# Kernel optimization log

Hardware: AMD Instinct MI355X
Metric: run time of the kernel (lower is better)

The kernel has to match this reference:

```python
import jax, jax.numpy as jnp
import numpy as np

BS, NPTS, NM, D = 8, 8192, 32, 512  # objects, points/object, masks/object, feature dim


def setup_inputs() -> dict:
    key = jax.random.key(0)
    k1, k2, k3 = jax.random.split(key, 3)
    net_out = jax.random.normal(k1, (BS * NPTS, D), dtype=jnp.float32)
    mask_embs = jax.random.normal(k2, (BS * NM, D), dtype=jnp.float32)
    mask_pts = (jax.random.uniform(k3, (BS, NM, NPTS)) < 0.5).astype(jnp.float32)
    pt_offset = (jnp.arange(1, BS + 1) * NPTS).astype(jnp.int32)  # per-object end idx
    logit_scale = jnp.float32(2.6593)  # ln(1/0.07), CLIP-style
    return {
        "net_out": net_out,
        "mask_embs": mask_embs,
        "mask_pts": mask_pts,
        "logit_scale": logit_scale,
        "pt_offset": pt_offset,
    }


def reference(net_out, mask_embs, mask_pts, logit_scale, pt_offset):
    bs, nm, npts = mask_pts.shape
    d = net_out.shape[1]
    n_total = bs * nm

    # ragged per-object mask_pt @ net_out[start:end] -> uniform batched matmul
    net = net_out.reshape(bs, npts, d)
    sum_feats = jnp.einsum('bmp,bpd->bmd', mask_pts, net).reshape(n_total, d)

    mask_npts = jnp.sum(mask_pts, axis=-1).reshape(n_total, 1)  # points per mask
    nopts = (mask_npts[:, 0] == 0)                              # empty masks -> ignored
    avg_feats = sum_feats / (mask_npts + 1e-12)

    logits = (mask_embs @ avg_feats.T) * jnp.exp(logit_scale)   # [N, N]

    idx = jnp.arange(n_total)
    valid = ~nopts  # target == -100 (ignore) for empty masks, else arange diagonal
    texts_loss = jnp.where(valid, -jax.nn.log_softmax(logits, axis=-1)[idx, idx], 0.0)
    pts_loss = jnp.where(valid, -jax.nn.log_softmax(logits.T, axis=-1)[idx, idx], 0.0)

    def nonzero_avg(l):
        cnt = jnp.sum(l > 0)
        return jnp.where(cnt > 0, jnp.sum(l) / jnp.maximum(cnt, 1), 0.0)

    return (nonzero_avg(texts_loss) + nonzero_avg(pts_loss)) / 2.0
```

## Files before the change

### kernel.cpp

```cpp
#include <hip/hip_runtime.h>
#include <hip/hip_bf16.h>
#include <math.h>

#define BS 8
#define NPTS 8192
#define NM 32
#define D 512
#define NT (BS*NM)
#define KC 32
#define KCHUNK (NPTS/KC)
#define TILES (KCHUNK/32)
#define DC 8
#define DCHUNK (D/DC)
#define NWORDS (NPTS/32)

#define LOG2E 1.44269504088896f
#define LN2   0.69314718055995f

typedef short short8 __attribute__((ext_vector_type(8)));
typedef float f32x4 __attribute__((ext_vector_type(4)));

static constexpr size_t OFF_SUMF = 0;
static constexpr size_t OFF_CNTS = OFF_SUMF + (size_t)NT*D;
static constexpr size_t OFF_BITS = OFF_CNTS + NT;
static constexpr size_t OFF_LOG  = OFF_BITS + (size_t)NT*NWORDS;
static constexpr size_t OFF_RLSE = OFF_LOG + (size_t)NT*NT;
static constexpr size_t OFF_CLSE = OFF_RLSE + NT;
static constexpr size_t OFF_TICK = OFF_CLSE + NT;

__device__ __forceinline__ short bf16_rne(float f) {
  return __builtin_bit_cast(short, __float2bfloat16(f));
}

#define GLOAD_LDS16(g, l) __builtin_amdgcn_global_load_lds( \
    (const __attribute__((address_space(1))) void*)(g),     \
    (__attribute__((address_space(3))) void*)(l), 16, 0, 0)

__global__ __launch_bounds__(256) void kp_prep(const float* __restrict__ mpts,
                                               unsigned int* __restrict__ mbits,
                                               float* __restrict__ cnts,
                                               float* __restrict__ sumf,
                                               int* __restrict__ ticket) {
  const int n = blockIdx.x;
  const int t = threadIdx.x;
  if (n == 0 && t == 0) *ticket = 0;
  const float4* mp = (const float4*)(mpts + ((size_t)n << 13) + t * 32);
  unsigned int u = 0;
  #pragma unroll
  for (int q = 0; q < 8; ++q) {
    const float4 v = mp[q];
    u |= (v.x != 0.f ? 1u : 0u) << (q * 4 + 0);
    u |= (v.y != 0.f ? 1u : 0u) << (q * 4 + 1);
    u |= (v.z != 0.f ? 1u : 0u) << (q * 4 + 2);
    u |= (v.w != 0.f ? 1u : 0u) << (q * 4 + 3);
  }
  mbits[n * NWORDS + t] = u;
  ((float2*)(sumf + ((size_t)n << 9)))[t] = make_float2(0.f, 0.f);
  int c = __popc(u);
  #pragma unroll
  for (int o = 32; o > 0; o >>= 1) c += __shfl_down(c, o, 64);
  __shared__ int red[4];
  if ((t & 63) == 0) red[t >> 6] = c;
  __syncthreads();
  if (t == 0) cnts[n] = (float)(red[0] + red[1] + red[2] + red[3]);
}

__global__ __launch_bounds__(256, 8) void k1_mfma(const float* __restrict__ net,
                                                  const unsigned int* __restrict__ mbits,
                                                  float* __restrict__ sumf) {
  __shared__ float tile[2][32 * DCHUNK];
  const int bx = blockIdx.x;
  const int dc = bx & 7;
  const int kc = (bx >> 3) & 31;
  const int b  = bx >> 8;
  const int w    = threadIdx.x >> 6;
  const int lane = threadIdx.x & 63;
  const int lhi = lane >> 4, llo = lane & 15;
  const int k0 = kc * KCHUNK;

  auto stage = [&](int buf, int t) {
    const int kt = k0 + t * 32;
    #pragma unroll
    for (int si = 0; si < 2; ++si) {
      const int s = w * 2 + si;
      const int gsrc = (lane & 15) ^ (((s >> 1) & 3) << 2);
      const float* src = net
        + (((size_t)(b * NPTS + kt + s * 4 + (lane >> 4))) << 9)
        + dc * DCHUNK + (gsrc << 2);
      GLOAD_LDS16(src, &tile[buf][s * 256]);
    }
  };

  const unsigned int* r0 = mbits + (size_t)(b * NM + llo) * NWORDS + kc * TILES;
  const unsigned int* r1 = r0 + (size_t)16 * NWORDS;

  f32x4 acc0 = {0.f, 0.f, 0.f, 0.f};
  f32x4 acc1 = {0.f, 0.f, 0.f, 0.f};

  const int rbase = (lhi * 8) * 64 + ((((w * 4) + (llo >> 2)) ^ (lhi << 2)) << 2) + (llo & 3);
  const int sh = lhi * 8;

  stage(0, 0);
  __syncthreads();

  #pragma unroll
  for (int t = 0; t < TILES; ++t) {
    const int cur = t & 1;
    const unsigned int u0 = r0[t];
    const unsigned int u1 = r1[t];
    if (t + 1 < TILES) stage(cur ^ 1, t + 1);

    float bv[8];
    #pragma unroll
    for (int j = 0; j < 8; ++j) bv[j] = tile[cur][rbase + j * 64];

    short8 bf, a0f, a1f;
    #pragma unroll
    for (int j = 0; j < 8; ++j) bf[j] = bf16_rne(bv[j]);
    const unsigned int b0 = (u0 >> sh) & 0xffu;
    const unsigned int b1 = (u1 >> sh) & 0xffu;
    #pragma unroll
    for (int j = 0; j < 8; ++j) {
      a0f[j] = (short)(-(int)((b0 >> j) & 1u) & 0x3F80);
      a1f[j] = (short)(-(int)((b1 >> j) & 1u) & 0x3F80);
    }

    acc0 = __builtin_amdgcn_mfma_f32_16x16x32_bf16(a0f, bf, acc0, 0, 0, 0);
    acc1 = __builtin_amdgcn_mfma_f32_16x16x32_bf16(a1f, bf, acc1, 0, 0, 0);

    __syncthreads();
  }

  const int d0 = dc * DCHUNK + w * 16;
  float* sp = sumf + (((size_t)(b * NM)) << 9) + d0 + llo;
  #pragma unroll
  for (int j = 0; j < 4; ++j) {
    atomicAdd(sp + ((size_t)(lhi * 4 + j) << 9),      acc0[j]);
    atomicAdd(sp + ((size_t)(16 + lhi * 4 + j) << 9), acc1[j]);
  }
}

__global__ __launch_bounds__(128) void k2_logits(const float* __restrict__ embs,
                                                 const float* __restrict__ sumf,
                                                 const float* __restrict__ cnts,
                                                 const float* __restrict__ lsc,
                                                 float* __restrict__ logits) {
  const int h = threadIdx.x >> 6;
  const int lane = threadIdx.x & 63;
  const int wt = blockIdx.x;
  const int ti = wt >> 4, tj = wt & 15;
  const int lhi = lane >> 4, llo = lane & 15;

  const float* ea = embs + (((size_t)(ti * 16 + llo)) << 9) + h * 256 + lhi * 8;
  const float* sv = sumf + (((size_t)(tj * 16 + llo)) << 9) + h * 256 + lhi * 8;
  f32x4 acc = {0.f, 0.f, 0.f, 0.f};
  #pragma unroll
  for (int kk = 0; kk < 8; ++kk) {
    const float4 e0 = *(const float4*)(ea);
    const float4 e1 = *(const float4*)(ea + 4);
    const float4 v0 = *(const float4*)(sv);
    const float4 v1 = *(const float4*)(sv + 4);
    const float ev[8] = {e0.x, e0.y, e0.z, e0.w, e1.x, e1.y, e1.z, e1.w};
    const float vv[8] = {v0.x, v0.y, v0.z, v0.w, v1.x, v1.y, v1.z, v1.w};
    short8 ef, vf;
    #pragma unroll
    for (int j = 0; j < 8; ++j) { ef[j] = bf16_rne(ev[j]); vf[j] = bf16_rne(vv[j]); }
    acc = __builtin_amdgcn_mfma_f32_16x16x32_bf16(ef, vf, acc, 0, 0, 0);
    ea += 32; sv += 32;
  }

  __shared__ float part[64 * 4];
  if (h == 1) *(float4*)(&part[lane * 4]) = make_float4(acc[0], acc[1], acc[2], acc[3]);
  __syncthreads();
  if (h == 0) {
    const float4 p = *(const float4*)(&part[lane * 4]);
    const float scale = expf(lsc[0]);
    const float invc = scale / (cnts[tj * 16 + llo] + 1e-12f);
    float* lp = logits + (size_t)(ti * 16) * NT + tj * 16 + llo;
    lp[(size_t)(lhi * 4 + 0) * NT] = (acc[0] + p.x) * invc;
    lp[(size_t)(lhi * 4 + 1) * NT] = (acc[1] + p.y) * invc;
    lp[(size_t)(lhi * 4 + 2) * NT] = (acc[2] + p.z) * invc;
    lp[(size_t)(lhi * 4 + 3) * NT] = (acc[3] + p.w) * invc;
  }
}

__global__ __launch_bounds__(256) void k3_lse(const float* __restrict__ logits,
                                              float* __restrict__ rowlse,
                                              float* __restrict__ clse,
                                              const float* __restrict__ cnts,
                                              int* __restrict__ ticket,
                                              float* __restrict__ out) {
  const int g = blockIdx.x;
  const int r = threadIdx.x >> 4;
  const int c = threadIdx.x & 15;
  __shared__ float red[16][17];
  if (g < 16) {
    const int col = g * 16 + c;
    float mx = -1e30f;
    #pragma unroll 4
    for (int kk = 0; kk < 16; ++kk)
      mx = fmaxf(mx, logits[(size_t)(kk * 16 + r) * NT + col]);
    red[r][c] = mx; __syncthreads();
    for (int st = 8; st; st >>= 1) { if (r < st) red[r][c] = fmaxf(red[r][c], red[r + st][c]); __syncthreads(); }
    const float mx2 = red[0][c] * LOG2E; __syncthreads();
    float s = 0.f;
    #pragma unroll 4
    for (int kk = 0; kk < 16; ++kk)
      s += exp2f(logits[(size_t)(kk * 16 + r) * NT + col] * LOG2E - mx2);
    red[r][c] = s; __syncthreads();
    for (int st = 8; st; st >>= 1) { if (r < st) red[r][c] += red[r + st][c]; __syncthreads(); }
    if (r == 0) clse[col] = (mx2 + log2f(red[0][c])) * LN2;
  } else {
    const int row = (g - 16) * 16 + r;
    float mx = -1e30f;
    #pragma unroll 4
    for (int kk = 0; kk < 16; ++kk)
      mx = fmaxf(mx, logits[(size_t)row * NT + kk * 16 + c]);
    #pragma unroll
    for (int o = 8; o; o >>= 1) mx = fmaxf(mx, __shfl_xor(mx, o, 64));
    const float mx2 = mx * LOG2E;
    float s = 0.f;
    #pragma unroll 4
    for (int kk = 0; kk < 16; ++kk)
      s += exp2f(logits[(size_t)row * NT + kk * 16 + c] * LOG2E - mx2);
    #pragma unroll
    for (int o = 8; o; o >>= 1) s += __shfl_xor(s, o, 64);
    if (c == 0) rowlse[row] = (mx2 + log2f(s)) * LN2;
  }

  __shared__ int slast;
  __syncthreads();
  if (threadIdx.x == 0) {
    __threadfence();
    slast = (atomicAdd(ticket, 1) == 31);
  }
  __syncthreads();
  if (!slast) return;
  __threadfence();

  const int i = threadIdx.x;
  const float diag = logits[(size_t)i * NT + i];
  const bool valid = cnts[i] > 0.f;
  const float tl = valid ? (rowlse[i] - diag) : 0.f;
  const float pl = valid ? (clse[i] - diag) : 0.f;

  __shared__ float fred[4][256];
  fred[0][i] = tl;
  fred[1][i] = (tl > 0.f) ? 1.f : 0.f;
  fred[2][i] = pl;
  fred[3][i] = (pl > 0.f) ? 1.f : 0.f;
  __syncthreads();
  for (int st = 128; st > 0; st >>= 1) {
    if (i < st) {
      fred[0][i] += fred[0][i + st];
      fred[1][i] += fred[1][i + st];
      fred[2][i] += fred[2][i + st];
      fred[3][i] += fred[3][i + st];
    }
    __syncthreads();
  }
  if (i == 0) {
    const float a1 = (fred[1][0] > 0.f) ? fred[0][0] / fmaxf(fred[1][0], 1.f) : 0.f;
    const float a2 = (fred[3][0] > 0.f) ? fred[2][0] / fmaxf(fred[3][0], 1.f) : 0.f;
    out[0] = 0.5f * (a1 + a2);
  }
}

extern "C" void kernel_launch(void* const* d_in, const int* in_sizes, int n_in,
                              void* d_out, int out_size, void* d_ws, size_t ws_size,
                              hipStream_t stream) {
  const float* net  = (const float*)d_in[0];
  const float* embs = (const float*)d_in[1];
  const float* mpts = (const float*)d_in[2];
  const float* lsc  = (const float*)d_in[3];

  float* ws     = (float*)d_ws;
  float* sumf   = ws + OFF_SUMF;
  float* cnts   = ws + OFF_CNTS;
  unsigned int* mbits = (unsigned int*)(ws + OFF_BITS);
  float* logits = ws + OFF_LOG;
  float* rowlse = ws + OFF_RLSE;
  float* clse   = ws + OFF_CLSE;
  int*   ticket = (int*)(ws + OFF_TICK);
  float* outp   = (float*)d_out;

  kp_prep<<<dim3(NT), dim3(256), 0, stream>>>(mpts, mbits, cnts, sumf, ticket);
  k1_mfma<<<dim3(BS * KC * DC), dim3(256), 0, stream>>>(net, mbits, sumf);
  k2_logits<<<dim3(NT), dim3(128), 0, stream>>>(embs, sumf, cnts, lsc, logits);
  k3_lse<<<dim3(32), dim3(256), 0, stream>>>(logits, rowlse, clse, cnts, ticket, outp);
}
```

Measured before the change: 51.95 us.

## Triple-buffer k1 LDS staging with vmcnt waits and ballot-based mask packing

The matmul kernel moves from double to triple buffering of the LDS tiles. It uses explicit s_waitcnt vmcnt plus a single barrier per iteration, replacing two __syncthreads, so global-to-LDS loads run two tiles ahead. Each lane's 8 mask words are preloaded with vector loads before the loop, and the occupancy hint drops from 8 to 6 to fit the larger LDS footprint. The prep kernel now packs mask bits with wave ballots over coalesced scalar loads instead of per-thread float4 loops, producing the same bit layout.

New measurement: 56.50 us. +8.8%, slower.

```diff
diff --git a/kernel.cpp b/kernel.cpp
--- a/kernel.cpp
+++ b/kernel.cpp
@@ -43,32 +43,31 @@
                                                int* __restrict__ ticket) {
   const int n = blockIdx.x;
   const int t = threadIdx.x;
+  const int w = t >> 6, lane = t & 63;
   if (n == 0 && t == 0) *ticket = 0;
-  const float4* mp = (const float4*)(mpts + ((size_t)n << 13) + t * 32);
-  unsigned int u = 0;
-  #pragma unroll
-  for (int q = 0; q < 8; ++q) {
-    const float4 v = mp[q];
-    u |= (v.x != 0.f ? 1u : 0u) << (q * 4 + 0);
-    u |= (v.y != 0.f ? 1u : 0u) << (q * 4 + 1);
-    u |= (v.z != 0.f ? 1u : 0u) << (q * 4 + 2);
-    u |= (v.w != 0.f ? 1u : 0u) << (q * 4 + 3);
-  }
-  mbits[n * NWORDS + t] = u;
+
+  const float* base = mpts + ((size_t)n << 13) + w * 2048;
+  uint2* wout = (uint2*)(mbits + (size_t)n * NWORDS + w * 64);
+  int cnt = 0;
+  #pragma unroll 8
+  for (int i = 0; i < 32; ++i) {
+    const float v = base[i * 64 + lane];
+    const unsigned long long m = __ballot(v != 0.f);
+    cnt += __popcll(m);
+    if (lane == 0) wout[i] = make_uint2((unsigned)m, (unsigned)(m >> 32));
+  }
+  __shared__ float redc[4];
+  if (lane == 0) redc[w] = (float)cnt;
+  __syncthreads();
+  if (t == 0) cnts[n] = redc[0] + redc[1] + redc[2] + redc[3];
+
   ((float2*)(sumf + ((size_t)n << 9)))[t] = make_float2(0.f, 0.f);
-  int c = __popc(u);
-  #pragma unroll
-  for (int o = 32; o > 0; o >>= 1) c += __shfl_down(c, o, 64);
-  __shared__ int red[4];
-  if ((t & 63) == 0) red[t >> 6] = c;
-  __syncthreads();
-  if (t == 0) cnts[n] = (float)(red[0] + red[1] + red[2] + red[3]);
-}
-
-__global__ __launch_bounds__(256, 8) void k1_mfma(const float* __restrict__ net,
+}
+
+__global__ __launch_bounds__(256, 6) void k1_mfma(const float* __restrict__ net,
                                                   const unsigned int* __restrict__ mbits,
                                                   float* __restrict__ sumf) {
-  __shared__ float tile[2][32 * DCHUNK];
+  __shared__ float tile[3][32 * DCHUNK];
   const int bx = blockIdx.x;
   const int dc = bx & 7;
   const int kc = (bx >> 3) & 31;
@@ -78,6 +77,15 @@
   const int lhi = lane >> 4, llo = lane & 15;
   const int k0 = kc * KCHUNK;
 
+  const unsigned int* r0p = mbits + (size_t)(b * NM + llo) * NWORDS + kc * TILES;
+  const unsigned int* r1p = r0p + (size_t)16 * NWORDS;
+  const uint4 ma = *(const uint4*)(r0p);
+  const uint4 mb = *(const uint4*)(r0p + 4);
+  const uint4 mc = *(const uint4*)(r1p);
+  const uint4 md = *(const uint4*)(r1p + 4);
+  const unsigned int w0[8] = {ma.x, ma.y, ma.z, ma.w, mb.x, mb.y, mb.z, mb.w};
+  const unsigned int w1[8] = {mc.x, mc.y, mc.z, mc.w, md.x, md.y, md.z, md.w};
+
   auto stage = [&](int buf, int t) {
     const int kt = k0 + t * 32;
     #pragma unroll
@@ -91,9 +99,6 @@
     }
   };
 
-  const unsigned int* r0 = mbits + (size_t)(b * NM + llo) * NWORDS + kc * TILES;
-  const unsigned int* r1 = r0 + (size_t)16 * NWORDS;
-
   f32x4 acc0 = {0.f, 0.f, 0.f, 0.f};
   f32x4 acc1 = {0.f, 0.f, 0.f, 0.f};
 
@@ -101,24 +106,27 @@
   const int sh = lhi * 8;
 
   stage(0, 0);
-  __syncthreads();
+  stage(1, 1);
 
   #pragma unroll
   for (int t = 0; t < TILES; ++t) {
-    const int cur = t & 1;
-    const unsigned int u0 = r0[t];
-    const unsigned int u1 = r1[t];
-    if (t + 1 < TILES) stage(cur ^ 1, t + 1);
+    if (t < TILES - 1) {
+      asm volatile("s_waitcnt vmcnt(2)" ::: "memory");
+    } else {
+      asm volatile("s_waitcnt vmcnt(0)" ::: "memory");
+    }
+    __builtin_amdgcn_s_barrier();
+    if (t + 2 < TILES) stage((t + 2) % 3, t + 2);
 
     float bv[8];
     #pragma unroll
-    for (int j = 0; j < 8; ++j) bv[j] = tile[cur][rbase + j * 64];
+    for (int j = 0; j < 8; ++j) bv[j] = tile[t % 3][rbase + j * 64];
 
     short8 bf, a0f, a1f;
     #pragma unroll
     for (int j = 0; j < 8; ++j) bf[j] = bf16_rne(bv[j]);
-    const unsigned int b0 = (u0 >> sh) & 0xffu;
-    const unsigned int b1 = (u1 >> sh) & 0xffu;
+    const unsigned int b0 = (w0[t] >> sh) & 0xffu;
+    const unsigned int b1 = (w1[t] >> sh) & 0xffu;
     #pragma unroll
     for (int j = 0; j < 8; ++j) {
       a0f[j] = (short)(-(int)((b0 >> j) & 1u) & 0x3F80);
@@ -127,8 +135,6 @@
 
     acc0 = __builtin_amdgcn_mfma_f32_16x16x32_bf16(a0f, bf, acc0, 0, 0, 0);
     acc1 = __builtin_amdgcn_mfma_f32_16x16x32_bf16(a1f, bf, acc1, 0, 0, 0);
-
-    __syncthreads();
   }
 
   const int d0 = dc * DCHUNK + w * 16;
```
